# Kernel optimization log

Measured on AMD Instinct MI355X. Metric: run time of the kernel, lower is better.

## Reference

```python
import jax, jax.numpy as jnp
import numpy as np

B, T, D, H = 64, 512, 300, 1024
EPS = 1e-5


def setup_inputs() -> dict:
    key = jax.random.key(0)
    ks = jax.random.split(key, 9)
    x = jax.random.normal(ks[0], (B, T, D), jnp.float32)
    t = jax.random.bernoulli(ks[1], 0.5, (B,)).astype(jnp.float32)
    # LockedDropout mask: Bernoulli(1-0.5) / (1-0.5), fixed across timesteps
    mask = jax.random.bernoulli(ks[2], 0.5, (B, H)).astype(jnp.float32) / 0.5
    s = 1.0 / np.sqrt(H)
    W_ih = jax.random.uniform(ks[3], (4 * H, D), jnp.float32, -s, s)
    W_hh = jax.random.uniform(ks[4], (4 * H, H), jnp.float32, -s, s)
    b_ih = jax.random.uniform(ks[5], (4 * H,), jnp.float32, -s, s)
    b_hh = jax.random.uniform(ks[6], (4 * H,), jnp.float32, -s, s)
    gamma = jnp.ones((H,), jnp.float32)
    beta = jnp.zeros((H,), jnp.float32)
    sf = 1.0 / np.sqrt(H)
    fc_w = jax.random.uniform(ks[7], (1, H), jnp.float32, -sf, sf)
    fc_b = jax.random.uniform(ks[8], (1,), jnp.float32, -sf, sf)
    return {"x": x, "t": t, "mask": mask, "W_ih": W_ih, "W_hh": W_hh,
            "b_ih": b_ih, "b_hh": b_hh, "gamma": gamma, "beta": beta,
            "fc_w": fc_w, "fc_b": fc_b}


def reference(x, t, mask, W_ih, W_hh, b_ih, b_hh, gamma, beta, fc_w, fc_b):
    Bs, Ts, _ = x.shape
    Hs = W_hh.shape[1]

    def step(carry, xt):  # xt: [B, D]
        h, c = carry
        gates = xt @ W_ih.T + b_ih + h @ W_hh.T + b_hh  # [B, 4H]
        i, f, g, o = jnp.split(gates, 4, axis=1)        # torch LSTMCell gate order
        c2 = jax.nn.sigmoid(f) * c + jax.nn.sigmoid(i) * jnp.tanh(g)
        h2 = jax.nn.sigmoid(o) * jnp.tanh(c2)           # raw LSTM state carried forward
        # BatchNorm1d in train mode: biased batch statistics
        mu = h2.mean(axis=0)
        var = h2.var(axis=0)
        hn = gamma * (h2 - mu) * jax.lax.rsqrt(var + EPS) + beta
        return (h2, c2), hn * mask                      # locked dropout, fixed mask

    h0 = jnp.zeros((Bs, Hs), x.dtype)
    c0 = jnp.zeros((Bs, Hs), x.dtype)
    _, outs = jax.lax.scan(step, (h0, c0), jnp.swapaxes(x, 0, 1))  # outs: [T, B, H]
    pooled = outs.max(axis=0)                            # MaxPool1d over all timesteps
    z = (pooled @ fc_w.T + fc_b)[:, 0]                   # [B] logits
    # BCEWithLogitsLoss (mean reduction), numerically stable
    loss = jnp.mean(jnp.logaddexp(0.0, z) - z * t)
    return (loss, z)
```

## Files before the change

### kernel.cpp

```cpp
#include <hip/hip_runtime.h>
#include <cstddef>
#include <cstdint>

#define BB 64
#define TT 512
#define HH 1024
#define DD 300
#define NTH 256
#define NBLK 128
#define HB 8
#define XPAD 320
#define KS_X 10
#define KS_H 32
#define BN_EPS 1e-5f

typedef short short8 __attribute__((ext_vector_type(8)));
typedef float f32x4 __attribute__((ext_vector_type(4)));
typedef unsigned u32x2 __attribute__((ext_vector_type(2)));

__device__ __forceinline__ float sigmoid_f(float v) {
  v = fminf(fmaxf(v, -30.f), 30.f);
  return 1.f / (1.f + __expf(-v));
}
__device__ __forceinline__ float tanh_f(float v) {
  float e = __expf(fminf(fmaxf(2.f * v, -30.f), 30.f));
  return (e - 1.f) / (e + 1.f);
}
__device__ __forceinline__ unsigned short tobf(float f) {
  unsigned u = __float_as_uint(f);
  u += 0x7fffu + ((u >> 16) & 1u);
  return (unsigned short)(u >> 16);
}

__device__ __forceinline__ void ldA_sc(const void* p, short8& d) {
  asm volatile("global_load_dwordx4 %0, %1, off sc0 sc1"
               : "=v"(d) : "v"(p) : "memory");
}
__device__ __forceinline__ void ldA_nc(const void* p, short8& d) {
  asm volatile("global_load_dwordx4 %0, %1, off"
               : "=v"(d) : "v"(p) : "memory");
}
__device__ __forceinline__ void ld4_sc(const void* p, f32x4& d) {
  asm volatile("global_load_dwordx4 %0, %1, off sc0 sc1"
               : "=v"(d) : "v"(p) : "memory");
}
__device__ __forceinline__ u32x2 ld2w_sc(const void* p) {
  u32x2 v;
  asm volatile("global_load_dwordx2 %0, %1, off sc0 sc1\n\ts_waitcnt vmcnt(0)"
               : "=v"(v) : "v"(p) : "memory");
  return v;
}
__device__ __forceinline__ void st_sc32(void* p, unsigned v) {
  asm volatile("global_store_dword %0, %1, off sc0 sc1\n\ts_waitcnt vmcnt(0)"
               :: "v"(p), "v"(v) : "memory");
}
#define WAITV(N)                                                   \
  do {                                                             \
    asm volatile("s_waitcnt vmcnt(" #N ")" ::: "memory");          \
    __builtin_amdgcn_sched_barrier(0);                             \
  } while (0)

__device__ __forceinline__ f32x4 mfma16(short8 a, short8 b, f32x4 c) {
  return __builtin_amdgcn_mfma_f32_16x16x32_bf16(a, b, c, 0, 0, 0);
}

__device__ __forceinline__ void poll_ge(const unsigned* slots, int tid, unsigned ep) {
  int it = 0;
  for (;;) {
    int ok = 1;
    if (tid < 64) {
      u32x2 v = ld2w_sc(&slots[2 * tid]);
      ok = (v.x >= ep && v.y >= ep) ? 1 : 0;
    }
    if (__syncthreads_and(ok)) break;
    if (++it > (1 << 20)) break;
    if (it > 1) __builtin_amdgcn_s_sleep(1);
  }
}

__global__ void init_k(unsigned* __restrict__ base, int ndw) {
  int idx = blockIdx.x * blockDim.x + threadIdx.x;
  for (int i = idx; i < ndw; i += gridDim.x * blockDim.x) st_sc32(base + i, 0u);
}

__global__ void xcvt_k(const float* __restrict__ x, unsigned short* __restrict__ xbf) {
  const int total = TT * BB * XPAD;
  for (int idx = blockIdx.x * blockDim.x + threadIdx.x; idx < total;
       idx += gridDim.x * blockDim.x) {
    int kx = idx % XPAD;
    int tb = idx / XPAD;
    int b = tb % BB, t = tb / BB;
    float v = (kx < DD) ? x[(size_t)b * (TT * DD) + (size_t)t * DD + kx] : 0.f;
    xbf[idx] = tobf(v);
  }
}

__global__ void __launch_bounds__(NTH, 1)
lstm_mfma(const float* __restrict__ Wih, const float* __restrict__ Whh,
          const float* __restrict__ bih, const float* __restrict__ bhh,
          const float* __restrict__ gammap, const float* __restrict__ betap,
          const float* __restrict__ maskp, const float* __restrict__ tlbl,
          const float* __restrict__ fcw, const float* __restrict__ fcb,
          const unsigned short* __restrict__ xbf, unsigned short* __restrict__ hbuf,
          float* __restrict__ partial, unsigned* __restrict__ slots,
          float* __restrict__ outp) {
  __shared__ short8 Wlds[2][KS_H + KS_X][64];
  __shared__ float Cs[64][33];
  __shared__ float red_s[4][64];

  const int tid = threadIdx.x;
  const int w = tid >> 6, l = tid & 63;
  const int blk = blockIdx.x;
  const int hb0 = blk * HB;

  for (int idx = tid; idx < 2 * (KS_H + KS_X) * 64; idx += NTH) {
    int nt = idx / ((KS_H + KS_X) * 64);
    int rem = idx % ((KS_H + KS_X) * 64);
    int ks = rem >> 6, ll = rem & 63;
    int colq = nt * 16 + (ll & 15);
    int g = colq >> 3, j = colq & 7;
    int r = g * HH + hb0 + j;
    int k0 = (ll >> 4) * 8;
    float v[8];
    if (ks < KS_H) {
      const float* src = Whh + (size_t)r * HH + ks * 32 + k0;
      f32x4 u0 = *(const f32x4*)src;
      f32x4 u1 = *(const f32x4*)(src + 4);
      v[0] = u0.x; v[1] = u0.y; v[2] = u0.z; v[3] = u0.w;
      v[4] = u1.x; v[5] = u1.y; v[6] = u1.z; v[7] = u1.w;
    } else {
      int d0 = (ks - KS_H) * 32 + k0;
#pragma unroll
      for (int e = 0; e < 8; ++e)
        v[e] = (d0 + e < DD) ? Wih[(size_t)r * DD + d0 + e] : 0.f;
    }
    short8 pk;
#pragma unroll
    for (int e = 0; e < 8; ++e) pk[e] = (short)tobf(v[e]);
    Wlds[nt][ks][ll] = pk;
  }

  const int row = w * 16 + (l & 15);
  const int lk16 = (l >> 4);

  const int b = l, j0 = 2 * w, j1 = 2 * w + 1;
  const float gam0 = gammap[hb0 + j0], gam1 = gammap[hb0 + j1];
  const float bet0 = betap[hb0 + j0], bet1 = betap[hb0 + j1];
  const float msk0 = maskp[(size_t)b * HH + hb0 + j0];
  const float msk1 = maskp[(size_t)b * HH + hb0 + j1];
  const float biI0 = bih[0 * HH + hb0 + j0] + bhh[0 * HH + hb0 + j0];
  const float biF0 = bih[1 * HH + hb0 + j0] + bhh[1 * HH + hb0 + j0];
  const float biG0 = bih[2 * HH + hb0 + j0] + bhh[2 * HH + hb0 + j0];
  const float biO0 = bih[3 * HH + hb0 + j0] + bhh[3 * HH + hb0 + j0];
  const float biI1 = bih[0 * HH + hb0 + j1] + bhh[0 * HH + hb0 + j1];
  const float biF1 = bih[1 * HH + hb0 + j1] + bhh[1 * HH + hb0 + j1];
  const float biG1 = bih[2 * HH + hb0 + j1] + bhh[2 * HH + hb0 + j1];
  const float biO1 = bih[3 * HH + hb0 + j1] + bhh[3 * HH + hb0 + j1];
  const float fw0 = fcw[hb0 + j0], fw1 = fcw[hb0 + j1];
  float creg0 = 0.f, creg1 = 0.f;
  float pool0 = -3.4e38f, pool1 = -3.4e38f;
  __syncthreads();

  for (int s = 0; s < TT; ++s) {
    const unsigned short* hc = hbuf + (size_t)(s & 1) * (BB * HH);
    unsigned short* hnx = hbuf + (size_t)((s + 1) & 1) * (BB * HH);

    const unsigned short* px = xbf + ((size_t)s * BB + row) * XPAD + lk16 * 8;
    short8 xa[KS_X];
#pragma unroll
    for (int i = 0; i < KS_X; ++i) ldA_nc(px + i * 32, xa[i]);
    WAITV(0);
    f32x4 acc0 = {0.f, 0.f, 0.f, 0.f}, acc1 = {0.f, 0.f, 0.f, 0.f};
#pragma unroll
    for (int i = 0; i < KS_X; ++i) {
      acc0 = mfma16(xa[i], Wlds[0][KS_H + i][l], acc0);
      acc1 = mfma16(xa[i], Wlds[1][KS_H + i][l], acc1);
    }

    poll_ge(slots, tid, (unsigned)s);

    const unsigned short* ph = hc + (size_t)lk16 * 512 + row * 8;
    short8 ha[KS_H];
#pragma unroll
    for (int i = 0; i < 8; ++i) ldA_sc(ph + i * 2048, ha[i]);
#pragma unroll
    for (int i = 8; i < 16; ++i) ldA_sc(ph + i * 2048, ha[i]);
    WAITV(8);
#pragma unroll
    for (int i = 16; i < 24; ++i) ldA_sc(ph + i * 2048, ha[i]);
#pragma unroll
    for (int i = 0; i < 8; ++i) {
      acc0 = mfma16(ha[i], Wlds[0][i][l], acc0);
      acc1 = mfma16(ha[i], Wlds[1][i][l], acc1);
    }
    WAITV(8);
#pragma unroll
    for (int i = 24; i < 32; ++i) ldA_sc(ph + i * 2048, ha[i]);
#pragma unroll
    for (int i = 8; i < 16; ++i) {
      acc0 = mfma16(ha[i], Wlds[0][i][l], acc0);
      acc1 = mfma16(ha[i], Wlds[1][i][l], acc1);
    }
    WAITV(8);
#pragma unroll
    for (int i = 16; i < 24; ++i) {
      acc0 = mfma16(ha[i], Wlds[0][i][l], acc0);
      acc1 = mfma16(ha[i], Wlds[1][i][l], acc1);
    }
    WAITV(0);
#pragma unroll
    for (int i = 24; i < 32; ++i) {
      acc0 = mfma16(ha[i], Wlds[0][i][l], acc0);
      acc1 = mfma16(ha[i], Wlds[1][i][l], acc1);
    }

    {
      int crow = w * 16 + (l >> 4) * 4;
      int cc0 = (l & 15), cc1 = 16 + (l & 15);
#pragma unroll
      for (int r = 0; r < 4; ++r) {
        Cs[crow + r][cc0] = acc0[r];
        Cs[crow + r][cc1] = acc1[r];
      }
    }
    __syncthreads();

    float gI0 = Cs[b][j0] + biI0, gF0 = Cs[b][8 + j0] + biF0;
    float gG0 = Cs[b][16 + j0] + biG0, gO0 = Cs[b][24 + j0] + biO0;
    float gI1 = Cs[b][j1] + biI1, gF1 = Cs[b][8 + j1] + biF1;
    float gG1 = Cs[b][16 + j1] + biG1, gO1 = Cs[b][24 + j1] + biO1;
    float c20 = sigmoid_f(gF0) * creg0 + sigmoid_f(gI0) * tanh_f(gG0);
    float h20 = sigmoid_f(gO0) * tanh_f(c20);
    float c21 = sigmoid_f(gF1) * creg1 + sigmoid_f(gI1) * tanh_f(gG1);
    float h21 = sigmoid_f(gO1) * tanh_f(c21);
    creg0 = c20;
    creg1 = c21;
    float s10 = h20, s20 = h20 * h20, s11 = h21, s21 = h21 * h21;
#pragma unroll
    for (int off = 32; off; off >>= 1) {
      s10 += __shfl_xor(s10, off, 64);
      s20 += __shfl_xor(s20, off, 64);
      s11 += __shfl_xor(s11, off, 64);
      s21 += __shfl_xor(s21, off, 64);
    }
    float mu0 = s10 * (1.f / 64.f), var0 = fmaf(-mu0, mu0, s20 * (1.f / 64.f));
    float mu1 = s11 * (1.f / 64.f), var1 = fmaf(-mu1, mu1, s21 * (1.f / 64.f));
    float hn0 = gam0 * (h20 - mu0) * rsqrtf(var0 + BN_EPS) + bet0;
    float hn1 = gam1 * (h21 - mu1) * rsqrtf(var1 + BN_EPS) + bet1;
    pool0 = fmaxf(pool0, hn0 * msk0);
    pool1 = fmaxf(pool1, hn1 * msk1);
    unsigned pk = (unsigned)tobf(h20) | ((unsigned)tobf(h21) << 16);
    st_sc32((unsigned*)(hnx + (size_t)blk * 512 + b * 8) + w, pk);
    __syncthreads();
    if (tid == 0) st_sc32(&slots[blk], (unsigned)(s + 1));
  }

  red_s[w][b] = pool0 * fw0 + pool1 * fw1;
  __syncthreads();
  if (tid < BB) {
    float part = red_s[0][tid] + red_s[1][tid] + red_s[2][tid] + red_s[3][tid];
    st_sc32(&partial[(size_t)tid * NBLK + blk], __float_as_uint(part));
  }
  __syncthreads();
  if (tid == 0) st_sc32(&slots[blk], (unsigned)(TT + 1));
  if (blk != 0) return;

  poll_ge(slots, tid, (unsigned)(TT + 1));
  {
    int fb = tid & 63, q = tid >> 6;
    const float* pp = partial + ((size_t)fb * NBLK + q * 32);
    f32x4 v0, v1, v2, v3, v4, v5, v6, v7;
    ld4_sc(pp + 0, v0);  ld4_sc(pp + 4, v1);  ld4_sc(pp + 8, v2);  ld4_sc(pp + 12, v3);
    ld4_sc(pp + 16, v4); ld4_sc(pp + 20, v5); ld4_sc(pp + 24, v6); ld4_sc(pp + 28, v7);
    WAITV(0);
    float sum = v0.x + v0.y + v0.z + v0.w + v1.x + v1.y + v1.z + v1.w +
                v2.x + v2.y + v2.z + v2.w + v3.x + v3.y + v3.z + v3.w +
                v4.x + v4.y + v4.z + v4.w + v5.x + v5.y + v5.z + v5.w +
                v6.x + v6.y + v6.z + v6.w + v7.x + v7.y + v7.z + v7.w;
    red_s[q][fb] = sum;
  }
  __syncthreads();
  if (tid < BB) {
    float z = red_s[0][tid] + red_s[1][tid] + red_s[2][tid] + red_s[3][tid] + fcb[0];
    outp[1 + tid] = z;
    float sp = fmaxf(z, 0.f) + log1pf(__expf(-fabsf(z)));
    float lt = sp - z * tlbl[tid];
#pragma unroll
    for (int off = 32; off; off >>= 1) lt += __shfl_xor(lt, off, 64);
    if (tid == 0) outp[0] = lt * (1.f / 64.f);
  }
}

extern "C" void kernel_launch(void* const* d_in, const int* in_sizes, int n_in,
                              void* d_out, int out_size, void* d_ws, size_t ws_size,
                              hipStream_t stream) {
  const float* x = (const float*)d_in[0];
  const float* tlbl = (const float*)d_in[1];
  const float* maskp = (const float*)d_in[2];
  const float* Wih = (const float*)d_in[3];
  const float* Whh = (const float*)d_in[4];
  const float* bih = (const float*)d_in[5];
  const float* bhh = (const float*)d_in[6];
  const float* gammap = (const float*)d_in[7];
  const float* betap = (const float*)d_in[8];
  const float* fcw = (const float*)d_in[9];
  const float* fcb = (const float*)d_in[10];
  float* outp = (float*)d_out;

  unsigned* slots = (unsigned*)d_ws;
  unsigned short* hbuf = (unsigned short*)((char*)d_ws + 4096);
  float* partial = (float*)((char*)d_ws + 4096 + 2 * BB * HH * 2);
  unsigned short* xbf =
      (unsigned short*)((char*)d_ws + 4096 + 2 * BB * HH * 2 + BB * NBLK * 4);

  int ndw = (4096 + BB * HH * 2) / 4;
  hipLaunchKernelGGL(init_k, dim3(64), dim3(NTH), 0, stream, (unsigned*)d_ws, ndw);
  hipLaunchKernelGGL(xcvt_k, dim3(2048), dim3(NTH), 0, stream, x, xbf);
  hipLaunchKernelGGL(lstm_mfma, dim3(NBLK), dim3(NTH), 0, stream,
                     Wih, Whh, bih, bhh, gammap, betap, maskp, tlbl, fcw, fcb,
                     xbf, hbuf, partial, slots, outp);
}
```

Measured before the change: 2.695 ms.

## Decouple batch-norm/pool from recurrence and use per-wave sync groups

The LSTM recurrence kernel now stores every timestep's bf16 hidden state to a full history buffer. Batch-norm statistics, the masked max-pool and the FC/loss move into separate kernels that run after the recurrence. Inside the recurrent loop each wave handles 16 batch rows and syncs only with its own slot group through a wave-level poll, which removes block-wide barriers and the LDS round trip for gates. Bias goes into the accumulator init and gate values are exchanged with shuffles. The cost is writing and re-reading about 64MB of history plus three extra kernel launches.

```diff
diff --git a/kernel.cpp b/kernel.cpp
--- a/kernel.cpp
+++ b/kernel.cpp
@@ -8,15 +8,18 @@
 #define DD 300
 #define NTH 256
 #define NBLK 128
-#define HB 8
+#define JB 8
+#define GB 16
 #define XPAD 320
 #define KS_X 10
 #define KS_H 32
+#define KS_T 42
 #define BN_EPS 1e-5f
 
 typedef short short8 __attribute__((ext_vector_type(8)));
 typedef float f32x4 __attribute__((ext_vector_type(4)));
 typedef unsigned u32x2 __attribute__((ext_vector_type(2)));
+typedef unsigned u32x4 __attribute__((ext_vector_type(4)));
 
 __device__ __forceinline__ float sigmoid_f(float v) {
   v = fminf(fmaxf(v, -30.f), 30.f);
@@ -31,6 +34,9 @@
   u += 0x7fffu + ((u >> 16) & 1u);
   return (unsigned short)(u >> 16);
 }
+__device__ __forceinline__ float bf2f(unsigned us) {
+  return __uint_as_float(us << 16);
+}
 
 __device__ __forceinline__ void ldA_sc(const void* p, short8& d) {
   asm volatile("global_load_dwordx4 %0, %1, off sc0 sc1"
@@ -40,8 +46,8 @@
   asm volatile("global_load_dwordx4 %0, %1, off"
                : "=v"(d) : "v"(p) : "memory");
 }
-__device__ __forceinline__ void ld4_sc(const void* p, f32x4& d) {
-  asm volatile("global_load_dwordx4 %0, %1, off sc0 sc1"
+__device__ __forceinline__ void ld2w_sc_nd(const void* p, u32x2& d) {
+  asm volatile("global_load_dwordx2 %0, %1, off sc0 sc1"
                : "=v"(d) : "v"(p) : "memory");
 }
 __device__ __forceinline__ u32x2 ld2w_sc(const void* p) {
@@ -54,6 +60,14 @@
   asm volatile("global_store_dword %0, %1, off sc0 sc1\n\ts_waitcnt vmcnt(0)"
                :: "v"(p), "v"(v) : "memory");
 }
+__device__ __forceinline__ void st_sc32_nd(void* p, unsigned v) {
+  asm volatile("global_store_dword %0, %1, off sc0 sc1"
+               :: "v"(p), "v"(v) : "memory");
+}
+__device__ __forceinline__ void st4_sc_nd(void* p, u32x4 v) {
+  asm volatile("global_store_dwordx4 %0, %1, off sc0 sc1"
+               :: "v"(p), "v"(v) : "memory");
+}
 #define WAITV(N)                                                   \
   do {                                                             \
     asm volatile("s_waitcnt vmcnt(" #N ")" ::: "memory");          \
@@ -64,23 +78,19 @@
   return __builtin_amdgcn_mfma_f32_16x16x32_bf16(a, b, c, 0, 0, 0);
 }
 
-__device__ __forceinline__ void poll_ge(const unsigned* slots, int tid, unsigned ep) {
+__device__ __forceinline__ void poll128(const unsigned* sl, int l, unsigned ep) {
   int it = 0;
   for (;;) {
-    int ok = 1;
-    if (tid < 64) {
-      u32x2 v = ld2w_sc(&slots[2 * tid]);
-      ok = (v.x >= ep && v.y >= ep) ? 1 : 0;
-    }
-    if (__syncthreads_and(ok)) break;
+    u32x2 v = ld2w_sc(&sl[2 * l]);
+    if (__all((v.x >= ep) && (v.y >= ep))) break;
     if (++it > (1 << 20)) break;
-    if (it > 1) __builtin_amdgcn_s_sleep(1);
-  }
-}
-
-__global__ void init_k(unsigned* __restrict__ base, int ndw) {
+    if (it > 2) __builtin_amdgcn_s_sleep(1);
+  }
+}
+
+__global__ void init_k(unsigned* __restrict__ slots) {
   int idx = blockIdx.x * blockDim.x + threadIdx.x;
-  for (int i = idx; i < ndw; i += gridDim.x * blockDim.x) st_sc32(base + i, 0u);
+  if (idx < 4 * NBLK) st_sc32(&slots[idx], 0u);
 }
 
 __global__ void xcvt_k(const float* __restrict__ x, unsigned short* __restrict__ xbf) {
@@ -96,199 +106,248 @@
 }
 
 __global__ void __launch_bounds__(NTH, 1)
-lstm_mfma(const float* __restrict__ Wih, const float* __restrict__ Whh,
-          const float* __restrict__ bih, const float* __restrict__ bhh,
-          const float* __restrict__ gammap, const float* __restrict__ betap,
-          const float* __restrict__ maskp, const float* __restrict__ tlbl,
-          const float* __restrict__ fcw, const float* __restrict__ fcb,
-          const unsigned short* __restrict__ xbf, unsigned short* __restrict__ hbuf,
-          float* __restrict__ partial, unsigned* __restrict__ slots,
-          float* __restrict__ outp) {
-  __shared__ short8 Wlds[2][KS_H + KS_X][64];
-  __shared__ float Cs[64][33];
-  __shared__ float red_s[4][64];
+lstm_k(const float* __restrict__ Wih, const float* __restrict__ Whh,
+       const float* __restrict__ bih, const float* __restrict__ bhh,
+       const unsigned short* __restrict__ xbf, unsigned short* __restrict__ hall,
+       unsigned* __restrict__ slots) {
+  __shared__ short8 Wlds[2][KS_T][64];
+  __shared__ unsigned short rep[4][GB][JB];
 
   const int tid = threadIdx.x;
-  const int w = tid >> 6, l = tid & 63;
-  const int blk = blockIdx.x;
-  const int hb0 = blk * HB;
-
-  for (int idx = tid; idx < 2 * (KS_H + KS_X) * 64; idx += NTH) {
-    int nt = idx / ((KS_H + KS_X) * 64);
-    int rem = idx % ((KS_H + KS_X) * 64);
+  const int g = tid >> 6, l = tid & 63;
+  const int blk = blockIdx.x, jb0 = blk * JB;
+
+  for (int idx = tid; idx < 2 * KS_T * 64; idx += NTH) {
+    int nt = idx / (KS_T * 64);
+    int rem = idx % (KS_T * 64);
     int ks = rem >> 6, ll = rem & 63;
-    int colq = nt * 16 + (ll & 15);
-    int g = colq >> 3, j = colq & 7;
-    int r = g * HH + hb0 + j;
+    int c = nt * 16 + (ll & 15);
+    int r = (c >> 3) * HH + jb0 + (c & 7);
     int k0 = (ll >> 4) * 8;
-    float v[8];
+    short8 pk;
     if (ks < KS_H) {
       const float* src = Whh + (size_t)r * HH + ks * 32 + k0;
       f32x4 u0 = *(const f32x4*)src;
       f32x4 u1 = *(const f32x4*)(src + 4);
-      v[0] = u0.x; v[1] = u0.y; v[2] = u0.z; v[3] = u0.w;
-      v[4] = u1.x; v[5] = u1.y; v[6] = u1.z; v[7] = u1.w;
+      pk[0] = (short)tobf(u0.x); pk[1] = (short)tobf(u0.y);
+      pk[2] = (short)tobf(u0.z); pk[3] = (short)tobf(u0.w);
+      pk[4] = (short)tobf(u1.x); pk[5] = (short)tobf(u1.y);
+      pk[6] = (short)tobf(u1.z); pk[7] = (short)tobf(u1.w);
     } else {
       int d0 = (ks - KS_H) * 32 + k0;
 #pragma unroll
       for (int e = 0; e < 8; ++e)
-        v[e] = (d0 + e < DD) ? Wih[(size_t)r * DD + d0 + e] : 0.f;
-    }
-    short8 pk;
-#pragma unroll
-    for (int e = 0; e < 8; ++e) pk[e] = (short)tobf(v[e]);
+        pk[e] = (d0 + e < DD) ? (short)tobf(Wih[(size_t)r * DD + d0 + e]) : (short)0;
+    }
     Wlds[nt][ks][ll] = pk;
   }
 
-  const int row = w * 16 + (l & 15);
-  const int lk16 = (l >> 4);
-
-  const int b = l, j0 = 2 * w, j1 = 2 * w + 1;
-  const float gam0 = gammap[hb0 + j0], gam1 = gammap[hb0 + j1];
-  const float bet0 = betap[hb0 + j0], bet1 = betap[hb0 + j1];
-  const float msk0 = maskp[(size_t)b * HH + hb0 + j0];
-  const float msk1 = maskp[(size_t)b * HH + hb0 + j1];
-  const float biI0 = bih[0 * HH + hb0 + j0] + bhh[0 * HH + hb0 + j0];
-  const float biF0 = bih[1 * HH + hb0 + j0] + bhh[1 * HH + hb0 + j0];
-  const float biG0 = bih[2 * HH + hb0 + j0] + bhh[2 * HH + hb0 + j0];
-  const float biO0 = bih[3 * HH + hb0 + j0] + bhh[3 * HH + hb0 + j0];
-  const float biI1 = bih[0 * HH + hb0 + j1] + bhh[0 * HH + hb0 + j1];
-  const float biF1 = bih[1 * HH + hb0 + j1] + bhh[1 * HH + hb0 + j1];
-  const float biG1 = bih[2 * HH + hb0 + j1] + bhh[2 * HH + hb0 + j1];
-  const float biO1 = bih[3 * HH + hb0 + j1] + bhh[3 * HH + hb0 + j1];
-  const float fw0 = fcw[hb0 + j0], fw1 = fcw[hb0 + j1];
-  float creg0 = 0.f, creg1 = 0.f;
-  float pool0 = -3.4e38f, pool1 = -3.4e38f;
+  const int cq = l & 15;
+  const float bc0 = bih[(cq >> 3) * HH + jb0 + (cq & 7)] +
+                    bhh[(cq >> 3) * HH + jb0 + (cq & 7)];
+  const float bc1 = bih[((cq >> 3) + 2) * HH + jb0 + (cq & 7)] +
+                    bhh[((cq >> 3) + 2) * HH + jb0 + (cq & 7)];
+  const int arow = g * GB + (l & 15);
+  const int lk16 = l >> 4;
+  const unsigned* slg = slots + g * NBLK;
+  unsigned* slg_w = slots + g * NBLK;
+
+  const int low = (cq < 8) ? 1 : 0;
+  const int jj = low ? cq : cq - 8;
+  const int sl0 = (l >> 4) * 4 + (low ? 0 : 2);
+  float cr0 = 0.f, cr1 = 0.f;
   __syncthreads();
 
   for (int s = 0; s < TT; ++s) {
-    const unsigned short* hc = hbuf + (size_t)(s & 1) * (BB * HH);
-    unsigned short* hnx = hbuf + (size_t)((s + 1) & 1) * (BB * HH);
-
-    const unsigned short* px = xbf + ((size_t)s * BB + row) * XPAD + lk16 * 8;
+    const unsigned short* px = xbf + ((size_t)s * BB + arow) * XPAD + lk16 * 8;
     short8 xa[KS_X];
-#pragma unroll
-    for (int i = 0; i < KS_X; ++i) ldA_nc(px + i * 32, xa[i]);
-    WAITV(0);
-    f32x4 acc0 = {0.f, 0.f, 0.f, 0.f}, acc1 = {0.f, 0.f, 0.f, 0.f};
+    if (s > 0) {
+      u32x2 pv;
+      ld2w_sc_nd(&slg[2 * l], pv);
+#pragma unroll
+      for (int i = 0; i < KS_X; ++i) ldA_nc(px + i * 32, xa[i]);
+      WAITV(10);
+      if (!__all((pv.x >= (unsigned)s) && (pv.y >= (unsigned)s)))
+        poll128(slg, l, (unsigned)s);
+    } else {
+#pragma unroll
+      for (int i = 0; i < KS_X; ++i) ldA_nc(px + i * 32, xa[i]);
+      WAITV(0);
+    }
+
+    short8 ha[KS_H];
+    if (s > 0) {
+      const unsigned short* ph =
+          hall + ((size_t)(s - 1) * BB + arow) * HH + lk16 * 8;
+#pragma unroll
+      for (int i = 0; i < KS_H; ++i) ldA_sc(ph + i * 32, ha[i]);
+      WAITV(32);
+    }
+
+    f32x4 acc0 = {bc0, bc0, bc0, bc0}, acc1 = {bc1, bc1, bc1, bc1};
 #pragma unroll
     for (int i = 0; i < KS_X; ++i) {
       acc0 = mfma16(xa[i], Wlds[0][KS_H + i][l], acc0);
       acc1 = mfma16(xa[i], Wlds[1][KS_H + i][l], acc1);
     }
-
-    poll_ge(slots, tid, (unsigned)s);
-
-    const unsigned short* ph = hc + (size_t)lk16 * 512 + row * 8;
-    short8 ha[KS_H];
-#pragma unroll
-    for (int i = 0; i < 8; ++i) ldA_sc(ph + i * 2048, ha[i]);
-#pragma unroll
-    for (int i = 8; i < 16; ++i) ldA_sc(ph + i * 2048, ha[i]);
-    WAITV(8);
-#pragma unroll
-    for (int i = 16; i < 24; ++i) ldA_sc(ph + i * 2048, ha[i]);
+    if (s > 0) {
+      WAITV(24);
+#pragma unroll
+      for (int i = 0; i < 8; ++i) {
+        acc0 = mfma16(ha[i], Wlds[0][i][l], acc0);
+        acc1 = mfma16(ha[i], Wlds[1][i][l], acc1);
+      }
+      WAITV(16);
+#pragma unroll
+      for (int i = 8; i < 16; ++i) {
+        acc0 = mfma16(ha[i], Wlds[0][i][l], acc0);
+        acc1 = mfma16(ha[i], Wlds[1][i][l], acc1);
+      }
+      WAITV(8);
+#pragma unroll
+      for (int i = 16; i < 24; ++i) {
+        acc0 = mfma16(ha[i], Wlds[0][i][l], acc0);
+        acc1 = mfma16(ha[i], Wlds[1][i][l], acc1);
+      }
+      WAITV(0);
+#pragma unroll
+      for (int i = 24; i < 32; ++i) {
+        acc0 = mfma16(ha[i], Wlds[0][i][l], acc0);
+        acc1 = mfma16(ha[i], Wlds[1][i][l], acc1);
+      }
+    }
+
+    f32x4 o0, o1;
+#pragma unroll
+    for (int r = 0; r < 4; ++r) {
+      o0[r] = __shfl_xor(acc0[r], 8, 64);
+      o1[r] = __shfl_xor(acc1[r], 8, 64);
+    }
+    {
+      int r0 = low ? 0 : 2, r1 = r0 + 1;
+      float gi0 = low ? acc0[r0] : o0[r0];
+      float gf0 = low ? o0[r0] : acc0[r0];
+      float gg0 = low ? acc1[r0] : o1[r0];
+      float go0 = low ? o1[r0] : acc1[r0];
+      float gi1 = low ? acc0[r1] : o0[r1];
+      float gf1 = low ? o0[r1] : acc0[r1];
+      float gg1 = low ? acc1[r1] : o1[r1];
+      float go1 = low ? o1[r1] : acc1[r1];
+      float c20 = sigmoid_f(gf0) * cr0 + sigmoid_f(gi0) * tanh_f(gg0);
+      float h20 = sigmoid_f(go0) * tanh_f(c20);
+      float c21 = sigmoid_f(gf1) * cr1 + sigmoid_f(gi1) * tanh_f(gg1);
+      float h21 = sigmoid_f(go1) * tanh_f(c21);
+      cr0 = c20;
+      cr1 = c21;
+      rep[g][sl0][jj] = tobf(h20);
+      rep[g][sl0 + 1][jj] = tobf(h21);
+    }
+    asm volatile("s_waitcnt lgkmcnt(0)" ::: "memory");
+    __builtin_amdgcn_sched_barrier(0);
+
+    if (l < GB) {
+      u32x4 pv = *(const u32x4*)&rep[g][l][0];
+      st4_sc_nd(hall + ((size_t)s * BB + g * GB + l) * HH + jb0, pv);
+    }
+    WAITV(0);
+    if (l == 0) st_sc32_nd(&slg_w[blk], (unsigned)(s + 1));
+  }
+}
+
+__global__ void __launch_bounds__(NTH, 4)
+stats_k(const unsigned short* __restrict__ hall, float* __restrict__ musig) {
+  int s = blockIdx.x, tid = threadIdx.x;
+  const unsigned short* base = hall + (size_t)s * BB * HH + tid * 4;
+  float sm0 = 0, sm1 = 0, sm2 = 0, sm3 = 0, q0 = 0, q1 = 0, q2 = 0, q3 = 0;
+  u32x2 v[8];
+  for (int b0 = 0; b0 < BB; b0 += 8) {
+#pragma unroll
+    for (int i = 0; i < 8; ++i) ld2w_sc_nd(base + (size_t)(b0 + i) * HH, v[i]);
+    WAITV(0);
 #pragma unroll
     for (int i = 0; i < 8; ++i) {
-      acc0 = mfma16(ha[i], Wlds[0][i][l], acc0);
-      acc1 = mfma16(ha[i], Wlds[1][i][l], acc1);
-    }
-    WAITV(8);
-#pragma unroll
-    for (int i = 24; i < 32; ++i) ldA_sc(ph + i * 2048, ha[i]);
-#pragma unroll
-    for (int i = 8; i < 16; ++i) {
-      acc0 = mfma16(ha[i], Wlds[0][i][l], acc0);
-      acc1 = mfma16(ha[i], Wlds[1][i][l], acc1);
-    }
-    WAITV(8);
-#pragma unroll
-    for (int i = 16; i < 24; ++i) {
-      acc0 = mfma16(ha[i], Wlds[0][i][l], acc0);
-      acc1 = mfma16(ha[i], Wlds[1][i][l], acc1);
-    }
+      float f0 = bf2f(v[i].x & 0xffffu), f1 = bf2f(v[i].x >> 16);
+      float f2 = bf2f(v[i].y & 0xffffu), f3 = bf2f(v[i].y >> 16);
+      sm0 += f0; q0 += f0 * f0;
+      sm1 += f1; q1 += f1 * f1;
+      sm2 += f2; q2 += f2 * f2;
+      sm3 += f3; q3 += f3 * f3;
+    }
+  }
+  float mu0 = sm0 * (1.f / 64.f), mu1 = sm1 * (1.f / 64.f);
+  float mu2 = sm2 * (1.f / 64.f), mu3 = sm3 * (1.f / 64.f);
+  f32x4 a = {mu0, rsqrtf(fmaf(-mu0, mu0, q0 * (1.f / 64.f)) + BN_EPS),
+             mu1, rsqrtf(fmaf(-mu1, mu1, q1 * (1.f / 64.f)) + BN_EPS)};
+  f32x4 b = {mu2, rsqrtf(fmaf(-mu2, mu2, q2 * (1.f / 64.f)) + BN_EPS),
+             mu3, rsqrtf(fmaf(-mu3, mu3, q3 * (1.f / 64.f)) + BN_EPS)};
+  float* o = musig + ((size_t)s * HH + tid * 4) * 2;
+  *(f32x4*)o = a;
+  *(f32x4*)(o + 4) = b;
+}
+
+__global__ void __launch_bounds__(NTH, 4)
+pool_k(const unsigned short* __restrict__ hall, const float* __restrict__ musig,
+       const float* __restrict__ gammap, const float* __restrict__ betap,
+       const float* __restrict__ maskp, const float* __restrict__ fcw,
+       const float* __restrict__ fcb, float* __restrict__ outp,
+       float* __restrict__ zbuf) {
+  __shared__ float red[4][64];
+  int b = blockIdx.x, tid = threadIdx.x;
+  int j0 = tid * 4;
+  float gm[4], bt[4], mk[4], fwv[4], pool[4];
+#pragma unroll
+  for (int i = 0; i < 4; ++i) {
+    gm[i] = gammap[j0 + i];
+    bt[i] = betap[j0 + i];
+    mk[i] = maskp[(size_t)b * HH + j0 + i];
+    fwv[i] = fcw[j0 + i];
+    pool[i] = -3.4e38f;
+  }
+  const unsigned short* hb = hall + (size_t)b * HH + j0;
+  u32x2 hv[8];
+  for (int s0 = 0; s0 < TT; s0 += 8) {
+#pragma unroll
+    for (int i = 0; i < 8; ++i)
+      ld2w_sc_nd(hb + (size_t)(s0 + i) * (BB * HH), hv[i]);
     WAITV(0);
 #pragma unroll
-    for (int i = 24; i < 32; ++i) {
-      acc0 = mfma16(ha[i], Wlds[0][i][l], acc0);
-      acc1 = mfma16(ha[i], Wlds[1][i][l], acc1);
-    }
-
-    {
-      int crow = w * 16 + (l >> 4) * 4;
-      int cc0 = (l & 15), cc1 = 16 + (l & 15);
-#pragma unroll
-      for (int r = 0; r < 4; ++r) {
-        Cs[crow + r][cc0] = acc0[r];
-        Cs[crow + r][cc1] = acc1[r];
-      }
-    }
-    __syncthreads();
-
-    float gI0 = Cs[b][j0] + biI0, gF0 = Cs[b][8 + j0] + biF0;
-    float gG0 = Cs[b][16 + j0] + biG0, gO0 = Cs[b][24 + j0] + biO0;
-    float gI1 = Cs[b][j1] + biI1, gF1 = Cs[b][8 + j1] + biF1;
-    float gG1 = Cs[b][16 + j1] + biG1, gO1 = Cs[b][24 + j1] + biO1;
-    float c20 = sigmoid_f(gF0) * creg0 + sigmoid_f(gI0) * tanh_f(gG0);
-    float h20 = sigmoid_f(gO0) * tanh_f(c20);
-    float c21 = sigmoid_f(gF1) * creg1 + sigmoid_f(gI1) * tanh_f(gG1);
-    float h21 = sigmoid_f(gO1) * tanh_f(c21);
-    creg0 = c20;
-    creg1 = c21;
-    float s10 = h20, s20 = h20 * h20, s11 = h21, s21 = h21 * h21;
-#pragma unroll
-    for (int off = 32; off; off >>= 1) {
-      s10 += __shfl_xor(s10, off, 64);
-      s20 += __shfl_xor(s20, off, 64);
-      s11 += __shfl_xor(s11, off, 64);
-      s21 += __shfl_xor(s21, off, 64);
-    }
-    float mu0 = s10 * (1.f / 64.f), var0 = fmaf(-mu0, mu0, s20 * (1.f / 64.f));
-    float mu1 = s11 * (1.f / 64.f), var1 = fmaf(-mu1, mu1, s21 * (1.f / 64.f));
-    float hn0 = gam0 * (h20 - mu0) * rsqrtf(var0 + BN_EPS) + bet0;
-    float hn1 = gam1 * (h21 - mu1) * rsqrtf(var1 + BN_EPS) + bet1;
-    pool0 = fmaxf(pool0, hn0 * msk0);
-    pool1 = fmaxf(pool1, hn1 * msk1);
-    unsigned pk = (unsigned)tobf(h20) | ((unsigned)tobf(h21) << 16);
-    st_sc32((unsigned*)(hnx + (size_t)blk * 512 + b * 8) + w, pk);
-    __syncthreads();
-    if (tid == 0) st_sc32(&slots[blk], (unsigned)(s + 1));
-  }
-
-  red_s[w][b] = pool0 * fw0 + pool1 * fw1;
+    for (int i = 0; i < 8; ++i) {
+      const float* ms = musig + ((size_t)(s0 + i) * HH + j0) * 2;
+      f32x4 m0 = *(const f32x4*)ms;
+      f32x4 m1 = *(const f32x4*)(ms + 4);
+      float f0 = bf2f(hv[i].x & 0xffffu), f1 = bf2f(hv[i].x >> 16);
+      float f2 = bf2f(hv[i].y & 0xffffu), f3 = bf2f(hv[i].y >> 16);
+      pool[0] = fmaxf(pool[0], (gm[0] * (f0 - m0.x) * m0.y + bt[0]) * mk[0]);
+      pool[1] = fmaxf(pool[1], (gm[1] * (f1 - m0.z) * m0.w + bt[1]) * mk[1]);
+      pool[2] = fmaxf(pool[2], (gm[2] * (f2 - m1.x) * m1.y + bt[2]) * mk[2]);
+      pool[3] = fmaxf(pool[3], (gm[3] * (f3 - m1.z) * m1.w + bt[3]) * mk[3]);
+    }
+  }
+  float part = pool[0] * fwv[0] + pool[1] * fwv[1] + pool[2] * fwv[2] +
+               pool[3] * fwv[3];
+  red[tid >> 6][tid & 63] = part;
   __syncthreads();
-  if (tid < BB) {
-    float part = red_s[0][tid] + red_s[1][tid] + red_s[2][tid] + red_s[3][tid];
-    st_sc32(&partial[(size_t)tid * NBLK + blk], __float_as_uint(part));
-  }
-  __syncthreads();
-  if (tid == 0) st_sc32(&slots[blk], (unsigned)(TT + 1));
-  if (blk != 0) return;
-
-  poll_ge(slots, tid, (unsigned)(TT + 1));
-  {
-    int fb = tid & 63, q = tid >> 6;
-    const float* pp = partial + ((size_t)fb * NBLK + q * 32);
-    f32x4 v0, v1, v2, v3, v4, v5, v6, v7;
-    ld4_sc(pp + 0, v0);  ld4_sc(pp + 4, v1);  ld4_sc(pp + 8, v2);  ld4_sc(pp + 12, v3);
-    ld4_sc(pp + 16, v4); ld4_sc(pp + 20, v5); ld4_sc(pp + 24, v6); ld4_sc(pp + 28, v7);
-    WAITV(0);
-    float sum = v0.x + v0.y + v0.z + v0.w + v1.x + v1.y + v1.z + v1.w +
-                v2.x + v2.y + v2.z + v2.w + v3.x + v3.y + v3.z + v3.w +
-                v4.x + v4.y + v4.z + v4.w + v5.x + v5.y + v5.z + v5.w +
-                v6.x + v6.y + v6.z + v6.w + v7.x + v7.y + v7.z + v7.w;
-    red_s[q][fb] = sum;
-  }
-  __syncthreads();
-  if (tid < BB) {
-    float z = red_s[0][tid] + red_s[1][tid] + red_s[2][tid] + red_s[3][tid] + fcb[0];
-    outp[1 + tid] = z;
-    float sp = fmaxf(z, 0.f) + log1pf(__expf(-fabsf(z)));
-    float lt = sp - z * tlbl[tid];
-#pragma unroll
-    for (int off = 32; off; off >>= 1) lt += __shfl_xor(lt, off, 64);
-    if (tid == 0) outp[0] = lt * (1.f / 64.f);
-  }
+  if (tid < 64) {
+    float v = red[0][tid] + red[1][tid] + red[2][tid] + red[3][tid];
+#pragma unroll
+    for (int off = 32; off; off >>= 1) v += __shfl_xor(v, off, 64);
+    if (tid == 0) {
+      float z = v + fcb[0];
+      outp[1 + b] = z;
+      zbuf[b] = z;
+    }
+  }
+}
+
+__global__ void loss_k(const float* __restrict__ zbuf,
+                       const float* __restrict__ tlbl, float* __restrict__ outp) {
+  int tid = threadIdx.x;
+  float z = zbuf[tid];
+  float sp = fmaxf(z, 0.f) + log1pf(__expf(-fabsf(z)));
+  float lt = sp - z * tlbl[tid];
+#pragma unroll
+  for (int off = 32; off; off >>= 1) lt += __shfl_xor(lt, off, 64);
+  if (tid == 0) outp[0] = lt * (1.f / 64.f);
 }
 
 extern "C" void kernel_launch(void* const* d_in, const int* in_sizes, int n_in,
@@ -308,15 +367,18 @@
   float* outp = (float*)d_out;
 
   unsigned* slots = (unsigned*)d_ws;
-  unsigned short* hbuf = (unsigned short*)((char*)d_ws + 4096);
-  float* partial = (float*)((char*)d_ws + 4096 + 2 * BB * HH * 2);
+  float* zbuf = (float*)((char*)d_ws + 2560);
+  unsigned short* hall = (unsigned short*)((char*)d_ws + 65536);
+  float* musig = (float*)((char*)d_ws + 65536 + (size_t)TT * BB * HH * 2);
   unsigned short* xbf =
-      (unsigned short*)((char*)d_ws + 4096 + 2 * BB * HH * 2 + BB * NBLK * 4);
-
-  int ndw = (4096 + BB * HH * 2) / 4;
-  hipLaunchKernelGGL(init_k, dim3(64), dim3(NTH), 0, stream, (unsigned*)d_ws, ndw);
+      (unsigned short*)((char*)musig + (size_t)TT * HH * 2 * sizeof(float));
+
+  hipLaunchKernelGGL(init_k, dim3(2), dim3(NTH), 0, stream, slots);
   hipLaunchKernelGGL(xcvt_k, dim3(2048), dim3(NTH), 0, stream, x, xbf);
-  hipLaunchKernelGGL(lstm_mfma, dim3(NBLK), dim3(NTH), 0, stream,
-                     Wih, Whh, bih, bhh, gammap, betap, maskp, tlbl, fcw, fcb,
-                     xbf, hbuf, partial, slots, outp);
-}
+  hipLaunchKernelGGL(lstm_k, dim3(NBLK), dim3(NTH), 0, stream,
+                     Wih, Whh, bih, bhh, xbf, hall, slots);
+  hipLaunchKernelGGL(stats_k, dim3(TT), dim3(NTH), 0, stream, hall, musig);
+  hipLaunchKernelGGL(pool_k, dim3(BB), dim3(NTH), 0, stream,
+                     hall, musig, gammap, betap, maskp, fcw, fcb, outp, zbuf);
+  hipLaunchKernelGGL(loss_k, dim3(1), dim3(64), 0, stream, zbuf, tlbl, outp);
+}
```

Result: slower. 5.213 ms (+93.4%).
